# Performance work log

Measured on AMD Instinct MI355X. Metric: run time of the kernel, lower is better.

## Reference

```python
import jax, jax.numpy as jnp
import numpy as np

NUM_GRAPHS = 64


def setup_inputs() -> dict:
    key = jax.random.key(0)
    ks = jax.random.split(key, 6)
    N, E, D, H = 100000, 1600000, 512, 128
    x = jax.random.normal(ks[0], (N, D), dtype=jnp.float32)
    edge_index = jax.random.randint(ks[1], (2, E), 0, N, dtype=jnp.int64)
    batch = jnp.sort(jax.random.randint(ks[2], (N,), 0, NUM_GRAPHS, dtype=jnp.int64))
    W1 = jax.random.normal(ks[3], (D, H), dtype=jnp.float32) * (1.0 / np.sqrt(D))
    b1 = jnp.zeros((H,), dtype=jnp.float32)
    W2 = jax.random.normal(ks[4], (H, H), dtype=jnp.float32) * (1.0 / np.sqrt(H))
    b2 = jnp.zeros((H,), dtype=jnp.float32)
    return {"x": x, "edge_index": edge_index, "batch": batch,
            "W1": W1, "b1": b1, "W2": W2, "b2": b2}


def _gcn_conv(x, row, col, norm, n_nodes, W, b):
    # PyG GCNConv: transform, then D^{-1/2}(A+I)D^{-1/2} propagate, then bias.
    h = x @ W                                   # [N, H]
    msg = h[row] * norm[:, None]                # gather + edge normalize
    out = jax.ops.segment_sum(msg, col, num_segments=n_nodes)  # scatter-add
    return out + b


def reference(x, edge_index, batch, W1, b1, W2, b2):
    N = x.shape[0]
    loop = jnp.arange(N, dtype=edge_index.dtype)
    row = jnp.concatenate([edge_index[0], loop])  # sources (with self loops)
    col = jnp.concatenate([edge_index[1], loop])  # targets
    deg = jax.ops.segment_sum(jnp.ones_like(col, dtype=x.dtype), col,
                              num_segments=N)
    dinv = jnp.where(deg > 0, jax.lax.rsqrt(deg), 0.0)
    norm = dinv[row] * dinv[col]

    h = jax.nn.relu(_gcn_conv(x, row, col, norm, N, W1, b1))
    h = jax.nn.relu(_gcn_conv(h, row, col, norm, N, W2, b2))

    # global_mean_pool over batch segment ids
    sums = jax.ops.segment_sum(h, batch, num_segments=NUM_GRAPHS)
    cnts = jax.ops.segment_sum(jnp.ones((N,), dtype=h.dtype), batch,
                               num_segments=NUM_GRAPHS)
    pooled = sums / jnp.maximum(cnts, 1.0)[:, None]
    # dropout is identity in eval mode
    return pooled
```

## Files before the change

### kernel.cpp

```cpp
#include <hip/hip_runtime.h>
#include <hip/hip_bf16.h>

typedef __attribute__((ext_vector_type(8))) short short8;
typedef __attribute__((ext_vector_type(4))) float f32x4;

__device__ __forceinline__ ushort f2b(float f) {
    union { float f; uint u; } v; v.f = f;
    uint u = v.u;
    u += 0x7fffu + ((u >> 16) & 1u);
    return (ushort)(u >> 16);
}
__device__ __forceinline__ float blo(uint u) { return __uint_as_float(u << 16); }
__device__ __forceinline__ float bhi(uint u) { return __uint_as_float(u & 0xffff0000u); }

__device__ __forceinline__ void gl_lds16(const void* g, void* s) {
    __builtin_amdgcn_global_load_lds(
        (const __attribute__((address_space(1))) void*)g,
        (__attribute__((address_space(3))) void*)s, 16, 0, 0);
}

#define ECAP 32768
#define CCAP 40960


__global__ __launch_bounds__(256) void k_setup_scatter(
    const float* __restrict__ W1, ushort* __restrict__ wt1b, int D,
    const float* __restrict__ W2, ushort* __restrict__ wt2b, int H,
    const int* __restrict__ batch, int N, int G, int* __restrict__ gstart,
    float* __restrict__ psum, float* __restrict__ dinv,
    uint* __restrict__ hb0zrow, uint* __restrict__ hb1zrow,
    const int* __restrict__ ei, int E, int NB, int* __restrict__ bcur,
    uint* __restrict__ ebuf, int c1b, int c2b, int bb) {
    __shared__ int h[128], gb[128], lc[128];
    int b = blockIdx.x, t = threadIdx.x;
    if (b < c1b) {
        int o = b * 256 + t;
        if (o < 128 * D) {
            int n = o / D, k = o - n * D;
            wt1b[o] = f2b(W1[(size_t)k * 128 + n]);
        }
    } else if (b < c1b + c2b) {
        int o = (b - c1b) * 256 + t;
        if (o < 128 * H) {
            int n = o / H, k = o - n * H;
            wt2b[o] = f2b(W2[(size_t)k * 128 + n]);
        }
    } else if (b < c1b + c2b + bb) {
        int i = (b - c1b - c2b) * 256 + t;
        if (i < N) {
            int bt = batch[i];
            int prev = (i == 0) ? -1 : batch[i - 1];
            for (int g = prev + 1; g <= bt; ++g) gstart[g] = i;
            if (i == N - 1)
                for (int g = bt + 1; g <= G; ++g) gstart[g] = N;
        }
    } else if (b == c1b + c2b + bb) {
        for (int i = t; i < G * H; i += 256) psum[i] = 0.f;
        if (t == 0) dinv[N] = 0.f;
        for (int i = t; i < 64; i += 256) { hb0zrow[i] = 0u; hb1zrow[i] = 0u; }
    } else {
        int sb = b - (c1b + c2b + bb + 1);
        if (t < 128) { h[t] = 0; lc[t] = 0; }
        __syncthreads();
        int e0 = sb * 2048;
        int r[8], c[8], bk[8];
#pragma unroll
        for (int u = 0; u < 8; ++u) {
            int e = e0 + u * 256 + t;
            if (e < E) {
                r[u] = ei[e];
                c[u] = ei[E + e];
                bk[u] = c[u] >> 10;
                atomicAdd(&h[bk[u]], 1);
            }
        }
        __syncthreads();
        if (t < NB && h[t]) gb[t] = atomicAdd(&bcur[t], h[t]);
        __syncthreads();
#pragma unroll
        for (int u = 0; u < 8; ++u) {
            int e = e0 + u * 256 + t;
            if (e < E) {
                int p = gb[bk[u]] + atomicAdd(&lc[bk[u]], 1);
                ebuf[(size_t)bk[u] * ECAP + p] = ((uint)(c[u] & 1023) << 22) | (uint)r[u];
            }
        }
    }
}


__global__ __launch_bounds__(256) void k_bucket_sort(const uint* __restrict__ ebuf,
                                                     const int* __restrict__ bcur,
                                                     int N, int NB,
                                                     uint* __restrict__ offs,
                                                     float* __restrict__ dinv,
                                                     int* __restrict__ csr) {
    __shared__ int cnt[1024];
    __shared__ int cur[1024];
    __shared__ int wsum[4];
    int t = threadIdx.x;
    int b = blockIdx.x;
    int node0 = b << 10;
    int nn = min(1024, N - node0);
    for (int i = t; i < nn; i += 256) cnt[i] = 0;
    __syncthreads();
    int e0 = b * ECAP, e1 = e0 + bcur[b];
    int e0p = b * CCAP;
    for (int e = e0 + t; e < e1; e += 256) atomicAdd(&cnt[ebuf[e] >> 22], 1);
    __syncthreads();
    int i0 = t * 4;
    int x[4], px[4];
#pragma unroll
    for (int j = 0; j < 4; ++j) {
        x[j] = (i0 + j < nn) ? cnt[i0 + j] : 0;
        px[j] = (x[j] + 7) & ~7;
    }
    int tot = px[0] + px[1] + px[2] + px[3];
    int run = tot;
    int lane = t & 63, w = t >> 6;
#pragma unroll
    for (int off = 1; off < 64; off <<= 1) {
        int v = __shfl_up(run, off);
        if (lane >= off) run += v;
    }
    if (lane == 63) wsum[w] = run;
    __syncthreads();
    int base = 0;
    for (int u = 0; u < w; ++u) base += wsum[u];
    base += run - tot;
#pragma unroll
    for (int j = 0; j < 4; ++j) {
        if (i0 + j < nn) {
            int node = node0 + i0 + j;
            offs[node] = ((uint)(e0p + base) << 10) | (uint)x[j];
            cur[i0 + j] = base;
            dinv[node] = rsqrtf((float)(x[j] + 1));
            for (int k = x[j]; k < px[j]; ++k) csr[e0p + base + k] = N;
            base += px[j];
        }
    }
    __syncthreads();
    for (int e = e0 + t; e < e1; e += 256) {
        uint v = ebuf[e];
        int p = atomicAdd(&cur[v >> 22], 1);
        csr[e0p + p] = (int)(v & 0x3FFFFFu);
    }
}


template <int NT>
__global__ __launch_bounds__(256) void k_gemm(
    const float* __restrict__ Ap, const ushort* __restrict__ Wt,
    const float* __restrict__ dinv, ushort* __restrict__ outb, int N) {
    constexpr int K = NT * 64;
    __shared__ __align__(16) char asb[128 * 64 * 4];
    __shared__ __align__(16) char bsb[128 * 64 * 2];
    const int tid = threadIdx.x;
    const int row0 = blockIdx.x * 128;
    const int w = tid >> 6, l = tid & 63;
    const int lr = l & 15, lk = l >> 4;
    f32x4 acc[2][8] = {};

    for (int t = 0; t < NT; ++t) {
        const int kb = t * 64;
        const char* A = (const char*)Ap;
#pragma unroll
        for (int i = 0; i < 8; ++i) {
            int b = (w << 13) + (i << 10) + (l << 4);
            int r = b >> 8, cb = b & 255;
            int sb = cb ^ ((r & 15) << 4);
            int gr = row0 + r;
            if (gr < N)
                gl_lds16(A + ((size_t)gr * K + kb) * 4 + sb,
                         asb + (w << 13) + (i << 10));
        }
#pragma unroll
        for (int i = 0; i < 4; ++i) {
            int b = (w << 12) + (i << 10) + (l << 4);
            int r = b >> 7, cb = b & 127;
            int sb = cb ^ ((r & 7) << 4);
            gl_lds16((const char*)Wt + ((size_t)r * K + kb) * 2 + sb,
                     bsb + (w << 12) + (i << 10));
        }
        __syncthreads();
        const int wr0 = w * 32;
#pragma unroll
        for (int ks = 0; ks < 2; ++ks) {
            short8 a0, a1;
            const int r0 = wr0 + lr, r1 = wr0 + 16 + lr;
            const int c0 = ks * 128 + lk * 32;
            float4 v00 = *(const float4*)(asb + (r0 << 8) + ((c0) ^ ((r0 & 15) << 4)));
            float4 v01 = *(const float4*)(asb + (r0 << 8) + ((c0 + 16) ^ ((r0 & 15) << 4)));
            float4 v10 = *(const float4*)(asb + (r1 << 8) + ((c0) ^ ((r1 & 15) << 4)));
            float4 v11 = *(const float4*)(asb + (r1 << 8) + ((c0 + 16) ^ ((r1 & 15) << 4)));
            a0[0] = (short)f2b(v00.x); a0[1] = (short)f2b(v00.y);
            a0[2] = (short)f2b(v00.z); a0[3] = (short)f2b(v00.w);
            a0[4] = (short)f2b(v01.x); a0[5] = (short)f2b(v01.y);
            a0[6] = (short)f2b(v01.z); a0[7] = (short)f2b(v01.w);
            a1[0] = (short)f2b(v10.x); a1[1] = (short)f2b(v10.y);
            a1[2] = (short)f2b(v10.z); a1[3] = (short)f2b(v10.w);
            a1[4] = (short)f2b(v11.x); a1[5] = (short)f2b(v11.y);
            a1[6] = (short)f2b(v11.z); a1[7] = (short)f2b(v11.w);
            const int c0b = ks * 64 + lk * 16;
#pragma unroll
            for (int nf = 0; nf < 8; ++nf) {
                const int nr = nf * 16 + lr;
                short8 bf = *(const short8*)(bsb + (nr << 7) + (c0b ^ ((nr & 7) << 4)));
                acc[0][nf] = __builtin_amdgcn_mfma_f32_16x16x32_bf16(a0, bf, acc[0][nf], 0, 0, 0);
                acc[1][nf] = __builtin_amdgcn_mfma_f32_16x16x32_bf16(a1, bf, acc[1][nf], 0, 0, 0);
            }
        }
        __syncthreads();
    }
#pragma unroll
    for (int mf = 0; mf < 2; ++mf) {
#pragma unroll
        for (int r = 0; r < 4; ++r) {
            int row = row0 + w * 32 + mf * 16 + lk * 4 + r;
            if (row < N) {
                float dv = dinv[row];
#pragma unroll
                for (int nf = 0; nf < 8; ++nf)
                    outb[(size_t)row * 128 + nf * 16 + lr] = f2b(acc[mf][nf][r] * dv);
            }
        }
    }
}


#define ACC8(v) { a[0] += blo(v.x); a[1] += bhi(v.x); a[2] += blo(v.y); a[3] += bhi(v.y); \
                  a[4] += blo(v.z); a[5] += bhi(v.z); a[6] += blo(v.w); a[7] += bhi(v.w); }


__global__ __launch_bounds__(256) void k_spmm_fuse(
    const uint4* __restrict__ hs4, const int* __restrict__ csr,
    const uint* __restrict__ offs, const float* __restrict__ dinv,
    const float* __restrict__ bias, const ushort* __restrict__ W2t,
    ushort* __restrict__ outb, int N) {
    __shared__ __align__(16) char hsb[16 * 256];
    __shared__ __align__(16) char wsb[128 * 256];
    const int tid = threadIdx.x;
    const int grp = tid >> 4, ql = tid & 15;
    const int node = blockIdx.x * 16 + grp;
    const bool active = node < N;
#pragma unroll
    for (int u = 0; u < 8; ++u) {
        int f = u * 256 + tid;
        int row = f >> 4, g = f & 15;
        *(uint4*)(wsb + row * 256 + ((g ^ (row & 15)) << 4)) =
            *(const uint4*)(W2t + (size_t)f * 8);
    }
    float a[8] = {};
    int beg = 0, pend = 0;
    if (active) {
        uint pv = offs[node];
        beg = (int)(pv >> 10);
        pend = beg + (((int)(pv & 1023u) + 7) & ~7);
        uint4 s = hs4[(size_t)node * 16 + ql];
        ACC8(s)
    }
    int i = beg;
    for (; i + 16 <= pend; i += 16) {
        int4 s0 = *(const int4*)(csr + i);
        int4 s1 = *(const int4*)(csr + i + 4);
        int4 s2 = *(const int4*)(csr + i + 8);
        int4 s3 = *(const int4*)(csr + i + 12);
        uint4 v0 = hs4[(size_t)s0.x * 16 + ql];
        uint4 v1 = hs4[(size_t)s0.y * 16 + ql];
        uint4 v2 = hs4[(size_t)s0.z * 16 + ql];
        uint4 v3 = hs4[(size_t)s0.w * 16 + ql];
        uint4 v4 = hs4[(size_t)s1.x * 16 + ql];
        uint4 v5 = hs4[(size_t)s1.y * 16 + ql];
        uint4 v6 = hs4[(size_t)s1.z * 16 + ql];
        uint4 v7 = hs4[(size_t)s1.w * 16 + ql];
        uint4 v8 = hs4[(size_t)s2.x * 16 + ql];
        uint4 v9 = hs4[(size_t)s2.y * 16 + ql];
        uint4 va = hs4[(size_t)s2.z * 16 + ql];
        uint4 vb = hs4[(size_t)s2.w * 16 + ql];
        uint4 vc = hs4[(size_t)s3.x * 16 + ql];
        uint4 vd = hs4[(size_t)s3.y * 16 + ql];
        uint4 ve = hs4[(size_t)s3.z * 16 + ql];
        uint4 vf = hs4[(size_t)s3.w * 16 + ql];
        ACC8(v0) ACC8(v1) ACC8(v2) ACC8(v3) ACC8(v4) ACC8(v5) ACC8(v6) ACC8(v7)
        ACC8(v8) ACC8(v9) ACC8(va) ACC8(vb) ACC8(vc) ACC8(vd) ACC8(ve) ACC8(vf)
    }
    if (i < pend) {
        int4 s0 = *(const int4*)(csr + i);
        int4 s1 = *(const int4*)(csr + i + 4);
        uint4 v0 = hs4[(size_t)s0.x * 16 + ql];
        uint4 v1 = hs4[(size_t)s0.y * 16 + ql];
        uint4 v2 = hs4[(size_t)s0.z * 16 + ql];
        uint4 v3 = hs4[(size_t)s0.w * 16 + ql];
        uint4 v4 = hs4[(size_t)s1.x * 16 + ql];
        uint4 v5 = hs4[(size_t)s1.y * 16 + ql];
        uint4 v6 = hs4[(size_t)s1.z * 16 + ql];
        uint4 v7 = hs4[(size_t)s1.w * 16 + ql];
        ACC8(v0) ACC8(v1) ACC8(v2) ACC8(v3) ACC8(v4) ACC8(v5) ACC8(v6) ACC8(v7)
    }
    uint4 hv = make_uint4(0u, 0u, 0u, 0u);
    if (active) {
        float dv = dinv[node];
        float4 b0 = ((const float4*)bias)[ql * 2];
        float4 b1v = ((const float4*)bias)[ql * 2 + 1];
        float o0 = fmaxf(fmaf(a[0], dv, b0.x), 0.f);
        float o1 = fmaxf(fmaf(a[1], dv, b0.y), 0.f);
        float o2 = fmaxf(fmaf(a[2], dv, b0.z), 0.f);
        float o3 = fmaxf(fmaf(a[3], dv, b0.w), 0.f);
        float o4 = fmaxf(fmaf(a[4], dv, b1v.x), 0.f);
        float o5 = fmaxf(fmaf(a[5], dv, b1v.y), 0.f);
        float o6 = fmaxf(fmaf(a[6], dv, b1v.z), 0.f);
        float o7 = fmaxf(fmaf(a[7], dv, b1v.w), 0.f);
        hv.x = ((uint)f2b(o1) << 16) | (uint)f2b(o0);
        hv.y = ((uint)f2b(o3) << 16) | (uint)f2b(o2);
        hv.z = ((uint)f2b(o5) << 16) | (uint)f2b(o4);
        hv.w = ((uint)f2b(o7) << 16) | (uint)f2b(o6);
    }
    *(uint4*)(hsb + grp * 256 + ((ql ^ grp) << 4)) = hv;
    __syncthreads();
    const int w = tid >> 6, l = tid & 63;
    const int lr = l & 15, lk = l >> 4;
    f32x4 acc[2] = {};
#pragma unroll
    for (int ks = 0; ks < 4; ++ks) {
        int g0 = ks * 4 + lk;
        short8 af = *(const short8*)(hsb + lr * 256 + ((g0 ^ lr) << 4));
#pragma unroll
        for (int j = 0; j < 2; ++j) {
            int nr = (w * 2 + j) * 16 + lr;
            short8 bf = *(const short8*)(wsb + nr * 256 + ((g0 ^ (nr & 15)) << 4));
            acc[j] = __builtin_amdgcn_mfma_f32_16x16x32_bf16(af, bf, acc[j], 0, 0, 0);
        }
    }
#pragma unroll
    for (int r = 0; r < 4; ++r) {
        int trow = lk * 4 + r;
        int onode = blockIdx.x * 16 + trow;
        if (onode < N) {
            float dv = dinv[onode];
#pragma unroll
            for (int j = 0; j < 2; ++j)
                outb[(size_t)onode * 128 + (w * 2 + j) * 16 + lr] = f2b(acc[j][r] * dv);
        }
    }
}


__global__ __launch_bounds__(256) void k_spmm_pool(
    const uint4* __restrict__ hs4, const int* __restrict__ csr,
    const uint* __restrict__ offs, const float* __restrict__ dinv,
    const float* __restrict__ bias,
    float* __restrict__ psum, const int* __restrict__ batch, int N) {
    __shared__ float4 pacc[16][32];
    __shared__ int gid[16];
    const int grp = threadIdx.x >> 4, ql = threadIdx.x & 15;
    const int node = blockIdx.x * 16 + grp;
    const bool active = node < N;
    float a[8] = {};
    int beg = 0, pend = 0;
    if (active) {
        uint pv = offs[node];
        beg = (int)(pv >> 10);
        pend = beg + (((int)(pv & 1023u) + 7) & ~7);
        uint4 s = hs4[(size_t)node * 16 + ql];
        ACC8(s)
    }
    int i = beg;
    for (; i + 16 <= pend; i += 16) {
        int4 s0 = *(const int4*)(csr + i);
        int4 s1 = *(const int4*)(csr + i + 4);
        int4 s2 = *(const int4*)(csr + i + 8);
        int4 s3 = *(const int4*)(csr + i + 12);
        uint4 v0 = hs4[(size_t)s0.x * 16 + ql];
        uint4 v1 = hs4[(size_t)s0.y * 16 + ql];
        uint4 v2 = hs4[(size_t)s0.z * 16 + ql];
        uint4 v3 = hs4[(size_t)s0.w * 16 + ql];
        uint4 v4 = hs4[(size_t)s1.x * 16 + ql];
        uint4 v5 = hs4[(size_t)s1.y * 16 + ql];
        uint4 v6 = hs4[(size_t)s1.z * 16 + ql];
        uint4 v7 = hs4[(size_t)s1.w * 16 + ql];
        uint4 v8 = hs4[(size_t)s2.x * 16 + ql];
        uint4 v9 = hs4[(size_t)s2.y * 16 + ql];
        uint4 va = hs4[(size_t)s2.z * 16 + ql];
        uint4 vb = hs4[(size_t)s2.w * 16 + ql];
        uint4 vc = hs4[(size_t)s3.x * 16 + ql];
        uint4 vd = hs4[(size_t)s3.y * 16 + ql];
        uint4 ve = hs4[(size_t)s3.z * 16 + ql];
        uint4 vf = hs4[(size_t)s3.w * 16 + ql];
        ACC8(v0) ACC8(v1) ACC8(v2) ACC8(v3) ACC8(v4) ACC8(v5) ACC8(v6) ACC8(v7)
        ACC8(v8) ACC8(v9) ACC8(va) ACC8(vb) ACC8(vc) ACC8(vd) ACC8(ve) ACC8(vf)
    }
    if (i < pend) {
        int4 s0 = *(const int4*)(csr + i);
        int4 s1 = *(const int4*)(csr + i + 4);
        uint4 v0 = hs4[(size_t)s0.x * 16 + ql];
        uint4 v1 = hs4[(size_t)s0.y * 16 + ql];
        uint4 v2 = hs4[(size_t)s0.z * 16 + ql];
        uint4 v3 = hs4[(size_t)s0.w * 16 + ql];
        uint4 v4 = hs4[(size_t)s1.x * 16 + ql];
        uint4 v5 = hs4[(size_t)s1.y * 16 + ql];
        uint4 v6 = hs4[(size_t)s1.z * 16 + ql];
        uint4 v7 = hs4[(size_t)s1.w * 16 + ql];
        ACC8(v0) ACC8(v1) ACC8(v2) ACC8(v3) ACC8(v4) ACC8(v5) ACC8(v6) ACC8(v7)
    }
    float o[8] = {};
    if (active) {
        float dv = dinv[node];
        float4 b0 = ((const float4*)bias)[ql * 2];
        float4 b1 = ((const float4*)bias)[ql * 2 + 1];
        o[0] = fmaxf(fmaf(a[0], dv, b0.x), 0.f);
        o[1] = fmaxf(fmaf(a[1], dv, b0.y), 0.f);
        o[2] = fmaxf(fmaf(a[2], dv, b0.z), 0.f);
        o[3] = fmaxf(fmaf(a[3], dv, b0.w), 0.f);
        o[4] = fmaxf(fmaf(a[4], dv, b1.x), 0.f);
        o[5] = fmaxf(fmaf(a[5], dv, b1.y), 0.f);
        o[6] = fmaxf(fmaf(a[6], dv, b1.z), 0.f);
        o[7] = fmaxf(fmaf(a[7], dv, b1.w), 0.f);
    }
    pacc[grp][ql * 2]     = make_float4(o[0], o[1], o[2], o[3]);
    pacc[grp][ql * 2 + 1] = make_float4(o[4], o[5], o[6], o[7]);
    if (ql == 0) gid[grp] = active ? batch[node] : -1;
    __syncthreads();
    int t = threadIdx.x;
    if (t < 128) {
        float run = 0.f; int prev = -1;
#pragma unroll
        for (int g2 = 0; g2 < 16; ++g2) {
            int g = gid[g2];
            if (g < 0) continue;
            if (g != prev && prev >= 0) { atomicAdd(&psum[prev * 128 + t], run); run = 0.f; }
            run += ((const float*)pacc[g2])[t];
            prev = g;
        }
        if (prev >= 0) atomicAdd(&psum[prev * 128 + t], run);
    }
}


__global__ void k_div(const float* __restrict__ psum, const int* __restrict__ gstart,
                      float* __restrict__ out, int total) {
    int i = blockIdx.x * blockDim.x + threadIdx.x;
    if (i < total) {
        int g = i >> 7;
        float c = (float)(gstart[g + 1] - gstart[g]);
        out[i] = psum[i] / fmaxf(c, 1.f);
    }
}


extern "C" void kernel_launch(void* const* d_in, const int* in_sizes, int n_in,
                              void* d_out, int out_size, void* d_ws, size_t ws_size,
                              hipStream_t stream) {
    const float* x     = (const float*)d_in[0];
    const int*   ei    = (const int*)d_in[1];
    const int*   batch = (const int*)d_in[2];
    const float* W1    = (const float*)d_in[3];
    const float* b1    = (const float*)d_in[4];
    const float* W2    = (const float*)d_in[5];
    const float* b2    = (const float*)d_in[6];
    float* outp = (float*)d_out;

    const int N = in_sizes[2];
    const int E = in_sizes[1] / 2;
    const int D = in_sizes[0] / N;
    const int H = in_sizes[4];
    const int G = out_size / H;
    const int NB = (N + 1023) >> 10;

    char* ws = (char*)d_ws;
    size_t off = 0;
    auto alloc = [&](size_t bytes) -> char* {
        char* p = ws + off;
        off = (off + bytes + 255) & ~(size_t)255;
        return p;
    };
    float*  dinv    = (float*)alloc((size_t)(N + 1) * 4);
    uint*   offs    = (uint*)alloc((size_t)N * 4);
    int*    gstart  = (int*)alloc((size_t)(G + 1) * 4);
    float*  psum    = (float*)alloc((size_t)G * H * 4);
    int*    bcur    = (int*)alloc(128 * 4);
    ushort* wt1b    = (ushort*)alloc((size_t)H * D * 2);
    ushort* wt2b    = (ushort*)alloc((size_t)H * H * 2);
    int*    csr     = (int*)alloc((size_t)NB * CCAP * 4);
    uint*   ebuf    = (uint*)alloc((size_t)NB * ECAP * 4);
    char*   hbase   = alloc((size_t)(N + 8) * 2 * H * 2);
    ushort* hb0     = (ushort*)hbase;
    ushort* hb1     = (ushort*)(hbase + ((size_t)N + 8) * H * 2);
    (void)ws_size; (void)n_in;

    hipMemsetAsync(bcur, 0, 128 * 4, stream);

    int c1b = (128 * D + 255) / 256;
    int c2b = (128 * H + 255) / 256;
    int bb  = (N + 255) / 256;
    int scb = (E + 2047) / 2048;

    k_setup_scatter<<<c1b + c2b + bb + 1 + scb, 256, 0, stream>>>(
        W1, wt1b, D, W2, wt2b, H, batch, N, G, gstart, psum, dinv,
        (uint*)(hb0 + (size_t)N * H), (uint*)(hb1 + (size_t)N * H),
        ei, E, NB, bcur, ebuf, c1b, c2b, bb);

    k_bucket_sort<<<NB, 256, 0, stream>>>(ebuf, bcur, N, NB, offs, dinv, csr);

    int gblocks = (N + 127) / 128;
    int sblocks = (N + 15) / 16;
    k_gemm<8><<<gblocks, 256, 0, stream>>>(x, wt1b, dinv, hb0, N);
    k_spmm_fuse<<<sblocks, 256, 0, stream>>>(
        (const uint4*)hb0, csr, offs, dinv, b1, wt2b, hb1, N);
    k_spmm_pool<<<sblocks, 256, 0, stream>>>(
        (const uint4*)hb1, csr, offs, dinv, b2, psum, batch, N);
    k_div<<<(G * H + 255) / 256, 256, 0, stream>>>(psum, gstart, outp, G * H);
}
```

Baseline: 251.3 us.

## Restructure first-layer GEMM with resident weights and per-wave double-buffered A pipeline

```diff
diff --git a/kernel.cpp b/kernel.cpp
--- a/kernel.cpp
+++ b/kernel.cpp
@@ -148,81 +148,107 @@
 }
 
 
-template <int NT>
-__global__ __launch_bounds__(256) void k_gemm(
-    const float* __restrict__ Ap, const ushort* __restrict__ Wt,
+__global__ __launch_bounds__(512) void k_gemm1_wi(
+    const float* __restrict__ A, const ushort* __restrict__ Wt,
     const float* __restrict__ dinv, ushort* __restrict__ outb, int N) {
-    constexpr int K = NT * 64;
-    __shared__ __align__(16) char asb[128 * 64 * 4];
-    __shared__ __align__(16) char bsb[128 * 64 * 2];
+    __shared__ __align__(16) char bsb[128 * 1024];
+    __shared__ __align__(16) char apv[8 * 4096];
     const int tid = threadIdx.x;
-    const int row0 = blockIdx.x * 128;
     const int w = tid >> 6, l = tid & 63;
     const int lr = l & 15, lk = l >> 4;
-    f32x4 acc[2][8] = {};
-
-    for (int t = 0; t < NT; ++t) {
-        const int kb = t * 64;
-        const char* A = (const char*)Ap;
-#pragma unroll
-        for (int i = 0; i < 8; ++i) {
-            int b = (w << 13) + (i << 10) + (l << 4);
-            int r = b >> 8, cb = b & 255;
-            int sb = cb ^ ((r & 15) << 4);
-            int gr = row0 + r;
+    const int row0 = blockIdx.x * 128;
+    const bool full = (row0 + 128 <= N);
+    f32x4 acc[8] = {};
+
+#pragma unroll
+    for (int i = 0; i < 16; ++i) {
+        int idx = i * 512 + tid;
+        int n = idx >> 6, g = idx & 63;
+        gl_lds16((const char*)Wt + n * 1024 + ((g ^ (n & 15)) << 4),
+                 bsb + i * 8192 + (tid << 4));
+    }
+
+    auto stageA = [&](int t) {
+        char* base = apv + w * 4096 + (t & 1) * 2048;
+#pragma unroll
+        for (int j = 0; j < 2; ++j) {
+            int idx = j * 64 + l;
+            int rl = idx >> 3, g = idx & 7;
+            gl_lds16((const char*)A + (size_t)(row0 + w * 16 + rl) * 2048 + t * 128 +
+                         ((g ^ (rl & 7)) << 4),
+                     base + j * 1024 + (l << 4));
+        }
+    };
+    auto stageA_g = [&](int t) {
+        char* base = apv + w * 4096 + (t & 1) * 2048;
+#pragma unroll
+        for (int j = 0; j < 2; ++j) {
+            int idx = j * 64 + l;
+            int rl = idx >> 3, g = idx & 7;
+            int gr = row0 + w * 16 + rl;
             if (gr < N)
-                gl_lds16(A + ((size_t)gr * K + kb) * 4 + sb,
-                         asb + (w << 13) + (i << 10));
-        }
-#pragma unroll
-        for (int i = 0; i < 4; ++i) {
-            int b = (w << 12) + (i << 10) + (l << 4);
-            int r = b >> 7, cb = b & 127;
-            int sb = cb ^ ((r & 7) << 4);
-            gl_lds16((const char*)Wt + ((size_t)r * K + kb) * 2 + sb,
-                     bsb + (w << 12) + (i << 10));
-        }
+                gl_lds16((const char*)A + (size_t)gr * 2048 + t * 128 +
+                             ((g ^ (rl & 7)) << 4),
+                         base + j * 1024 + (l << 4));
+        }
+    };
+    auto consume = [&](int t) {
+        const char* ab = apv + w * 4096 + (t & 1) * 2048 + lr * 128;
+        int x0 = (2 * lk) ^ (lr & 7);
+        int x1 = (2 * lk + 1) ^ (lr & 7);
+        float4 v0 = *(const float4*)(ab + (x0 << 4));
+        float4 v1 = *(const float4*)(ab + (x1 << 4));
+        short8 a;
+        a[0] = (short)f2b(v0.x); a[1] = (short)f2b(v0.y);
+        a[2] = (short)f2b(v0.z); a[3] = (short)f2b(v0.w);
+        a[4] = (short)f2b(v1.x); a[5] = (short)f2b(v1.y);
+        a[6] = (short)f2b(v1.z); a[7] = (short)f2b(v1.w);
+#pragma unroll
+        for (int nf = 0; nf < 8; ++nf) {
+            int nr = nf * 16 + lr;
+            short8 bf = *(const short8*)(bsb + nr * 1024 +
+                                         (((t * 4 + lk) ^ (nr & 15)) << 4));
+            acc[nf] = __builtin_amdgcn_mfma_f32_16x16x32_bf16(a, bf, acc[nf], 0, 0, 0);
+        }
+    };
+
+    if (full) {
+        stageA(0);
+        stageA(1);
+        asm volatile("s_waitcnt vmcnt(4)" ::: "memory");
         __syncthreads();
-        const int wr0 = w * 32;
-#pragma unroll
-        for (int ks = 0; ks < 2; ++ks) {
-            short8 a0, a1;
-            const int r0 = wr0 + lr, r1 = wr0 + 16 + lr;
-            const int c0 = ks * 128 + lk * 32;
-            float4 v00 = *(const float4*)(asb + (r0 << 8) + ((c0) ^ ((r0 & 15) << 4)));
-            float4 v01 = *(const float4*)(asb + (r0 << 8) + ((c0 + 16) ^ ((r0 & 15) << 4)));
-            float4 v10 = *(const float4*)(asb + (r1 << 8) + ((c0) ^ ((r1 & 15) << 4)));
-            float4 v11 = *(const float4*)(asb + (r1 << 8) + ((c0 + 16) ^ ((r1 & 15) << 4)));
-            a0[0] = (short)f2b(v00.x); a0[1] = (short)f2b(v00.y);
-            a0[2] = (short)f2b(v00.z); a0[3] = (short)f2b(v00.w);
-            a0[4] = (short)f2b(v01.x); a0[5] = (short)f2b(v01.y);
-            a0[6] = (short)f2b(v01.z); a0[7] = (short)f2b(v01.w);
-            a1[0] = (short)f2b(v10.x); a1[1] = (short)f2b(v10.y);
-            a1[2] = (short)f2b(v10.z); a1[3] = (short)f2b(v10.w);
-            a1[4] = (short)f2b(v11.x); a1[5] = (short)f2b(v11.y);
-            a1[6] = (short)f2b(v11.z); a1[7] = (short)f2b(v11.w);
-            const int c0b = ks * 64 + lk * 16;
-#pragma unroll
-            for (int nf = 0; nf < 8; ++nf) {
-                const int nr = nf * 16 + lr;
-                short8 bf = *(const short8*)(bsb + (nr << 7) + (c0b ^ ((nr & 7) << 4)));
-                acc[0][nf] = __builtin_amdgcn_mfma_f32_16x16x32_bf16(a0, bf, acc[0][nf], 0, 0, 0);
-                acc[1][nf] = __builtin_amdgcn_mfma_f32_16x16x32_bf16(a1, bf, acc[1][nf], 0, 0, 0);
+#pragma unroll
+        for (int t = 0; t < 16; ++t) {
+            if (t < 15) { asm volatile("s_waitcnt vmcnt(2)" ::: "memory"); }
+            else        { asm volatile("s_waitcnt vmcnt(0)" ::: "memory"); }
+            consume(t);
+            if (t + 2 < 16) {
+                asm volatile("s_waitcnt lgkmcnt(0)" ::: "memory");
+                stageA(t + 2);
             }
         }
+    } else {
+        stageA_g(0);
+        asm volatile("s_waitcnt vmcnt(0)" ::: "memory");
         __syncthreads();
-    }
-#pragma unroll
-    for (int mf = 0; mf < 2; ++mf) {
-#pragma unroll
-        for (int r = 0; r < 4; ++r) {
-            int row = row0 + w * 32 + mf * 16 + lk * 4 + r;
-            if (row < N) {
-                float dv = dinv[row];
-#pragma unroll
-                for (int nf = 0; nf < 8; ++nf)
-                    outb[(size_t)row * 128 + nf * 16 + lr] = f2b(acc[mf][nf][r] * dv);
+#pragma unroll
+        for (int t = 0; t < 16; ++t) {
+            consume(t);
+            if (t + 1 < 16) {
+                asm volatile("s_waitcnt lgkmcnt(0)" ::: "memory");
+                stageA_g(t + 1);
+                asm volatile("s_waitcnt vmcnt(0)" ::: "memory");
             }
+        }
+    }
+#pragma unroll
+    for (int r = 0; r < 4; ++r) {
+        int grow = row0 + w * 16 + lk * 4 + r;
+        if (grow < N) {
+            float dv = dinv[grow];
+#pragma unroll
+            for (int nf = 0; nf < 8; ++nf)
+                outb[(size_t)grow * 128 + nf * 16 + lr] = f2b(acc[nf][r] * dv);
         }
     }
 }
@@ -503,7 +529,7 @@
 
     int gblocks = (N + 127) / 128;
     int sblocks = (N + 15) / 16;
-    k_gemm<8><<<gblocks, 256, 0, stream>>>(x, wt1b, dinv, hb0, N);
+    k_gemm1_wi<<<gblocks, 512, 0, stream>>>(x, wt1b, dinv, hb0, N);
     k_spmm_fuse<<<sblocks, 256, 0, stream>>>(
         (const uint4*)hb0, csr, offs, dinv, b1, wt2b, hb1, N);
     k_spmm_pool<<<sblocks, 256, 0, stream>>>(
```

New measurement: 266.4 us. 6.0% more time.

## Fuse bucket sort into GEMM launch and compute degrees via global atomics

Applied to the files above, without the earlier changes.

```diff
diff --git a/kernel.cpp b/kernel.cpp
--- a/kernel.cpp
+++ b/kernel.cpp
@@ -30,7 +30,7 @@
     float* __restrict__ psum, float* __restrict__ dinv,
     uint* __restrict__ hb0zrow, uint* __restrict__ hb1zrow,
     const int* __restrict__ ei, int E, int NB, int* __restrict__ bcur,
-    uint* __restrict__ ebuf, int c1b, int c2b, int bb) {
+    int* __restrict__ cnt, uint* __restrict__ ebuf, int c1b, int c2b, int bb) {
     __shared__ int h[128], gb[128], lc[128];
     int b = blockIdx.x, t = threadIdx.x;
     if (b < c1b) {
@@ -72,6 +72,7 @@
                 c[u] = ei[E + e];
                 bk[u] = c[u] >> 10;
                 atomicAdd(&h[bk[u]], 1);
+                atomicAdd(&cnt[c[u]], 1);
             }
         }
         __syncthreads();
@@ -89,73 +90,72 @@
 }
 
 
-__global__ __launch_bounds__(256) void k_bucket_sort(const uint* __restrict__ ebuf,
-                                                     const int* __restrict__ bcur,
-                                                     int N, int NB,
-                                                     uint* __restrict__ offs,
-                                                     float* __restrict__ dinv,
-                                                     int* __restrict__ csr) {
-    __shared__ int cnt[1024];
-    __shared__ int cur[1024];
-    __shared__ int wsum[4];
-    int t = threadIdx.x;
-    int b = blockIdx.x;
-    int node0 = b << 10;
-    int nn = min(1024, N - node0);
-    for (int i = t; i < nn; i += 256) cnt[i] = 0;
-    __syncthreads();
-    int e0 = b * ECAP, e1 = e0 + bcur[b];
-    int e0p = b * CCAP;
-    for (int e = e0 + t; e < e1; e += 256) atomicAdd(&cnt[ebuf[e] >> 22], 1);
-    __syncthreads();
-    int i0 = t * 4;
-    int x[4], px[4];
-#pragma unroll
-    for (int j = 0; j < 4; ++j) {
-        x[j] = (i0 + j < nn) ? cnt[i0 + j] : 0;
-        px[j] = (x[j] + 7) & ~7;
-    }
-    int tot = px[0] + px[1] + px[2] + px[3];
-    int run = tot;
-    int lane = t & 63, w = t >> 6;
-#pragma unroll
-    for (int off = 1; off < 64; off <<= 1) {
-        int v = __shfl_up(run, off);
-        if (lane >= off) run += v;
-    }
-    if (lane == 63) wsum[w] = run;
-    __syncthreads();
-    int base = 0;
-    for (int u = 0; u < w; ++u) base += wsum[u];
-    base += run - tot;
-#pragma unroll
-    for (int j = 0; j < 4; ++j) {
-        if (i0 + j < nn) {
-            int node = node0 + i0 + j;
-            offs[node] = ((uint)(e0p + base) << 10) | (uint)x[j];
-            cur[i0 + j] = base;
-            dinv[node] = rsqrtf((float)(x[j] + 1));
-            for (int k = x[j]; k < px[j]; ++k) csr[e0p + base + k] = N;
-            base += px[j];
-        }
-    }
-    __syncthreads();
-    for (int e = e0 + t; e < e1; e += 256) {
-        uint v = ebuf[e];
-        int p = atomicAdd(&cur[v >> 22], 1);
-        csr[e0p + p] = (int)(v & 0x3FFFFFu);
-    }
-}
-
-
 template <int NT>
-__global__ __launch_bounds__(256) void k_gemm(
+__global__ __launch_bounds__(256) void k_gemm_sort(
     const float* __restrict__ Ap, const ushort* __restrict__ Wt,
-    const float* __restrict__ dinv, ushort* __restrict__ outb, int N) {
+    const int* __restrict__ cnt, ushort* __restrict__ outb, int N, int gblocks,
+    const uint* __restrict__ ebuf, const int* __restrict__ bcur, int NB,
+    uint* __restrict__ offs, float* __restrict__ dinv, int* __restrict__ csr) {
     constexpr int K = NT * 64;
-    __shared__ __align__(16) char asb[128 * 64 * 4];
-    __shared__ __align__(16) char bsb[128 * 64 * 2];
+    __shared__ __align__(16) char smem[128 * 64 * 4 + 128 * 64 * 2];
     const int tid = threadIdx.x;
+
+    if ((int)blockIdx.x >= gblocks) {
+        int* cnt_s = (int*)smem;
+        int* cur_s = (int*)(smem + 4096);
+        int* wsum  = (int*)(smem + 8192);
+        int t = tid;
+        int b = blockIdx.x - gblocks;
+        int node0 = b << 10;
+        int nn = min(1024, N - node0);
+        for (int i = t; i < nn; i += 256) cnt_s[i] = 0;
+        __syncthreads();
+        int e0 = b * ECAP, e1 = e0 + bcur[b];
+        int e0p = b * CCAP;
+        for (int e = e0 + t; e < e1; e += 256) atomicAdd(&cnt_s[ebuf[e] >> 22], 1);
+        __syncthreads();
+        int i0 = t * 4;
+        int x[4], px[4];
+#pragma unroll
+        for (int j = 0; j < 4; ++j) {
+            x[j] = (i0 + j < nn) ? cnt_s[i0 + j] : 0;
+            px[j] = (x[j] + 7) & ~7;
+        }
+        int tot = px[0] + px[1] + px[2] + px[3];
+        int run = tot;
+        int lane = t & 63, w = t >> 6;
+#pragma unroll
+        for (int off = 1; off < 64; off <<= 1) {
+            int v = __shfl_up(run, off);
+            if (lane >= off) run += v;
+        }
+        if (lane == 63) wsum[w] = run;
+        __syncthreads();
+        int base = 0;
+        for (int u = 0; u < w; ++u) base += wsum[u];
+        base += run - tot;
+#pragma unroll
+        for (int j = 0; j < 4; ++j) {
+            if (i0 + j < nn) {
+                int node = node0 + i0 + j;
+                offs[node] = ((uint)(e0p + base) << 10) | (uint)x[j];
+                cur_s[i0 + j] = base;
+                dinv[node] = rsqrtf((float)(x[j] + 1));
+                for (int k = x[j]; k < px[j]; ++k) csr[e0p + base + k] = N;
+                base += px[j];
+            }
+        }
+        __syncthreads();
+        for (int e = e0 + t; e < e1; e += 256) {
+            uint v = ebuf[e];
+            int p = atomicAdd(&cur_s[v >> 22], 1);
+            csr[e0p + p] = (int)(v & 0x3FFFFFu);
+        }
+        return;
+    }
+
+    char* asb = smem;
+    char* bsb = smem + 128 * 64 * 4;
     const int row0 = blockIdx.x * 128;
     const int w = tid >> 6, l = tid & 63;
     const int lr = l & 15, lk = l >> 4;
@@ -218,7 +218,7 @@
         for (int r = 0; r < 4; ++r) {
             int row = row0 + w * 32 + mf * 16 + lk * 4 + r;
             if (row < N) {
-                float dv = dinv[row];
+                float dv = rsqrtf((float)(cnt[row] + 1));
 #pragma unroll
                 for (int nf = 0; nf < 8; ++nf)
                     outb[(size_t)row * 128 + nf * 16 + lr] = f2b(acc[mf][nf][r] * dv);
@@ -478,6 +478,7 @@
     int*    gstart  = (int*)alloc((size_t)(G + 1) * 4);
     float*  psum    = (float*)alloc((size_t)G * H * 4);
     int*    bcur    = (int*)alloc(128 * 4);
+    int*    cnt     = (int*)alloc((size_t)(N + 1) * 4);
     ushort* wt1b    = (ushort*)alloc((size_t)H * D * 2);
     ushort* wt2b    = (ushort*)alloc((size_t)H * H * 2);
     int*    csr     = (int*)alloc((size_t)NB * CCAP * 4);
@@ -487,7 +488,7 @@
     ushort* hb1     = (ushort*)(hbase + ((size_t)N + 8) * H * 2);
     (void)ws_size; (void)n_in;
 
-    hipMemsetAsync(bcur, 0, 128 * 4, stream);
+    hipMemsetAsync(bcur, 0, (size_t)((char*)(cnt + N + 1) - (char*)bcur), stream);
 
     int c1b = (128 * D + 255) / 256;
     int c2b = (128 * H + 255) / 256;
@@ -497,13 +498,12 @@
     k_setup_scatter<<<c1b + c2b + bb + 1 + scb, 256, 0, stream>>>(
         W1, wt1b, D, W2, wt2b, H, batch, N, G, gstart, psum, dinv,
         (uint*)(hb0 + (size_t)N * H), (uint*)(hb1 + (size_t)N * H),
-        ei, E, NB, bcur, ebuf, c1b, c2b, bb);
-
-    k_bucket_sort<<<NB, 256, 0, stream>>>(ebuf, bcur, N, NB, offs, dinv, csr);
+        ei, E, NB, bcur, cnt, ebuf, c1b, c2b, bb);
 
     int gblocks = (N + 127) / 128;
     int sblocks = (N + 15) / 16;
-    k_gemm<8><<<gblocks, 256, 0, stream>>>(x, wt1b, dinv, hb0, N);
+    k_gemm_sort<8><<<gblocks + NB, 256, 0, stream>>>(
+        x, wt1b, cnt, hb0, N, gblocks, ebuf, bcur, NB, offs, dinv, csr);
     k_spmm_fuse<<<sblocks, 256, 0, stream>>>(
         (const uint4*)hb0, csr, offs, dinv, b1, wt2b, hb1, N);
     k_spmm_pool<<<sblocks, 256, 0, stream>>>(
```

Measured after the change: 295.6 us. 17.6% more time.
